# Kernel tuning notes

Hardware: AMD Instinct MI355X
Metric: run time of the kernel (lower is better)

The kernel has to match this reference:

```python
import jax, jax.numpy as jnp
import numpy as np

B, N, C, H, D = 1, 256, 128, 4, 32  # batch, n_res, c_z, heads, head_dim
LN_EPS = 1e-5


def setup_inputs() -> dict:
    key = jax.random.key(0)
    ks = jax.random.split(key, 10)
    s = 0.02
    return {
        "act": jax.random.normal(ks[0], (B, N, N, C), dtype=jnp.float32),
        "mask": jnp.ones((B, N, N), dtype=jnp.float32),
        "ln_g": jnp.ones((C,), dtype=jnp.float32),
        "ln_b": jnp.zeros((C,), dtype=jnp.float32),
        "w2d": jax.random.normal(ks[1], (C, H), dtype=jnp.float32) * s,
        "wq": jax.random.normal(ks[2], (C, H, D), dtype=jnp.float32) * s,
        "wk": jax.random.normal(ks[3], (C, H, D), dtype=jnp.float32) * s,
        "wv": jax.random.normal(ks[4], (C, H, D), dtype=jnp.float32) * s,
        "wg": jax.random.normal(ks[5], (C, H, D), dtype=jnp.float32) * s,
        "bg": jnp.ones((H, D), dtype=jnp.float32),
        "wo": jax.random.normal(ks[6], (H, D, C), dtype=jnp.float32) * s,
        "bo": jnp.zeros((C,), dtype=jnp.float32),
    }


def reference(act, mask, ln_g, ln_b, w2d, wq, wk, wv, wg, bg, wo, bo):
    # LayerNorm over channel dim
    mu = jnp.mean(act, axis=-1, keepdims=True)
    var = jnp.mean(jnp.square(act - mu), axis=-1, keepdims=True)
    x = (act - mu) * jax.lax.rsqrt(var + LN_EPS) * ln_g + ln_b  # [B,N,N,C]

    # mask bias: [B, I, 1, 1, K]
    mask_bias = (1e9 * (mask - 1.0))[:, :, None, None, :]
    # nonbatched pair bias: [B, 1, H, Q, K]
    nb_bias = jnp.einsum('bqkc,ch->bhqk', x, w2d)[:, None]

    scale = 1.0 / jnp.sqrt(jnp.asarray(D, dtype=x.dtype))
    q = jnp.einsum('bijc,chd->bijhd', x, wq) * scale  # [B,I,Q,H,D]
    k = jnp.einsum('bijc,chd->bijhd', x, wk)
    v = jnp.einsum('bijc,chd->bijhd', x, wv)

    logits = jnp.einsum('biqhd,bikhd->bihqk', q, k) + mask_bias + nb_bias
    a = jax.nn.softmax(logits, axis=-1)  # [B,I,H,Q,K]
    o = jnp.einsum('bihqk,bikhd->biqhd', a, v)  # [B,I,Q,H,D]

    g = jax.nn.sigmoid(jnp.einsum('bijc,chd->bijhd', x, wg) + bg)
    o = o * g
    out = jnp.einsum('biqhd,hdc->biqc', o, wo) + bo  # [B,N,N,C]
    return out
```

## Files before the change

kernel.cpp:

```cpp
#include <hip/hip_runtime.h>

#define QK_SCALE 0.17677669529663689f

typedef float f4 __attribute__((ext_vector_type(4)));
typedef short bf16x8 __attribute__((ext_vector_type(8)));
typedef float f32x4 __attribute__((ext_vector_type(4)));
typedef unsigned short us4 __attribute__((ext_vector_type(4)));
typedef unsigned int u32x2 __attribute__((ext_vector_type(2)));
typedef unsigned int u32x4 __attribute__((ext_vector_type(4)));

__device__ __forceinline__ unsigned short f2bf(float x){
  unsigned int u = __float_as_uint(x);
  u += 0x7fffu + ((u >> 16) & 1u);
  return (unsigned short)(u >> 16);
}
__device__ __forceinline__ float bf2f(unsigned short h){
  return __uint_as_float(((unsigned int)h) << 16);
}
__device__ __forceinline__ unsigned int cvtpk(float lo, float hi){
  unsigned int r;
  asm volatile("v_cvt_pk_bf16_f32 %0, %1, %2" : "=v"(r) : "v"(lo), "v"(hi));
  return r;
}
__device__ __forceinline__ f32x4 mfma16(bf16x8 a, bf16x8 b, f32x4 c){
  return __builtin_amdgcn_mfma_f32_16x16x32_bf16(a, b, c, 0, 0, 0);
}
__device__ __forceinline__ void gload_lds16(const void* g, void* s){
  __builtin_amdgcn_global_load_lds(
      (const __attribute__((address_space(1))) unsigned int*)g,
      (__attribute__((address_space(3))) unsigned int*)s, 16, 0, 0);
}

__global__ __launch_bounds__(256)
void k_prep(const float* __restrict__ wq, const float* __restrict__ wk,
            const float* __restrict__ wv, const float* __restrict__ wg,
            const float* __restrict__ wo, unsigned short* __restrict__ pk)
{
  const int m = blockIdx.x;
  const float* W = (m==0)? wq : (m==1)? wk : (m==2)? wv : (m==3)? wg : wo;
  const float scale = (m==0)? QK_SCALE : 1.0f;
  unsigned short* dst = pk + (long)m * 32768;
  for (int ent = threadIdx.x; ent < 2048; ent += 256){
    const int l = ent & 63, ktn = ent >> 6;
    const int kt = ktn & 3, nt = ktn >> 2;
    unsigned short* ph = dst + ((nt*4 + kt)*2 + 0)*512 + l*8;
    unsigned short* pl = dst + ((nt*4 + kt)*2 + 1)*512 + l*8;
    #pragma unroll
    for (int e = 0; e < 8; ++e){
      const int row = kt*32 + (l>>4)*8 + e;
      const int col = nt*16 + (l&15);
      float v = W[row*128 + col] * scale;
      unsigned short hh = f2bf(v);
      ph[e] = hh;
      pl[e] = f2bf(v - bf2f(hh));
    }
  }
}

__global__ __launch_bounds__(512, 4)
void k_proj(const float* __restrict__ act, const float* __restrict__ ln_g,
            const float* __restrict__ ln_b, const float* __restrict__ w2d,
            const unsigned short* __restrict__ pk, const float* __restrict__ bg,
            unsigned short* __restrict__ qf, unsigned short* __restrict__ kf,
            unsigned short* __restrict__ vt, unsigned short* __restrict__ gg,
            unsigned short* __restrict__ b2dh)
{
  __shared__ unsigned short afr[8*4*2*512];
  __shared__ unsigned short sc[4*640];
  const int t = threadIdx.x, w = t>>6, l = t&63, g16 = l>>4, c = l&15;
  const long p0 = (long)blockIdx.x * 128;
  const int bi = (int)(p0 >> 8);
  const int qb0 = (int)(p0 & 255);
  const int row = w*16 + c;

  {
    const float* ap = act + (p0 + row)*128;
    f4 xv[4][2];
    #pragma unroll
    for (int kt = 0; kt < 4; ++kt){
      xv[kt][0] = *(const f4*)(ap + kt*32 + g16*8);
      xv[kt][1] = *(const f4*)(ap + kt*32 + g16*8 + 4);
    }
    float s = 0.f, s2 = 0.f;
    #pragma unroll
    for (int kt = 0; kt < 4; ++kt)
      #pragma unroll
      for (int u = 0; u < 2; ++u)
        #pragma unroll
        for (int e = 0; e < 4; ++e){
          float x = xv[kt][u][e]; s += x; s2 += x*x;
        }
    s += __shfl_xor(s,16); s2 += __shfl_xor(s2,16);
    s += __shfl_xor(s,32); s2 += __shfl_xor(s2,32);
    const float mu = s*(1.f/128.f);
    const float iv = rsqrtf(fmaxf(s2*(1.f/128.f)-mu*mu,0.f)+1e-5f);

    float pb0=0.f, pb1=0.f, pb2=0.f, pb3=0.f;
    #pragma unroll
    for (int kt = 0; kt < 4; ++kt){
      bf16x8 hv, lv;
      #pragma unroll
      for (int u = 0; u < 2; ++u){
        const int cb = kt*32 + g16*8 + u*4;
        f4 lg = *(const f4*)(ln_g + cb);
        f4 lb = *(const f4*)(ln_b + cb);
        #pragma unroll
        for (int e0 = 0; e0 < 4; ++e0){
          float vv = (xv[kt][u][e0]-mu)*iv*lg[e0] + lb[e0];
          f4 wp = *(const f4*)(w2d + (cb+e0)*4);
          pb0 += vv*wp[0]; pb1 += vv*wp[1]; pb2 += vv*wp[2]; pb3 += vv*wp[3];
          unsigned short hh = f2bf(vv);
          hv[u*4+e0] = (short)hh;
          lv[u*4+e0] = (short)f2bf(vv - bf2f(hh));
        }
      }
      *(bf16x8*)&afr[((w*4+kt)*2+0)*512 + l*8] = hv;
      *(bf16x8*)&afr[((w*4+kt)*2+1)*512 + l*8] = lv;
    }
    pb0 += __shfl_xor(pb0,16); pb1 += __shfl_xor(pb1,16);
    pb2 += __shfl_xor(pb2,16); pb3 += __shfl_xor(pb3,16);
    pb0 += __shfl_xor(pb0,32); pb1 += __shfl_xor(pb1,32);
    pb2 += __shfl_xor(pb2,32); pb3 += __shfl_xor(pb3,32);
    const float pbsel = (g16==0)? pb0 : (g16==1)? pb1 : (g16==2)? pb2 : pb3;
    b2dh[g16*65536 + (int)p0 + row] = f2bf(pbsel);
  }
  __syncthreads();

  #pragma unroll
  for (int pass = 0; pass < 2; ++pass){
    bf16x8 bh0[4], bl0[4], bh1[4], bl1[4];
    { const int ntg = w*4 + pass*2;
      #pragma unroll
      for (int kt = 0; kt < 4; ++kt){
        bh0[kt] = *(const bf16x8*)(pk + ((ntg*4+kt)*2+0)*512 + l*8);
        bl0[kt] = *(const bf16x8*)(pk + ((ntg*4+kt)*2+1)*512 + l*8);
        bh1[kt] = *(const bf16x8*)(pk + (((ntg+1)*4+kt)*2+0)*512 + l*8);
        bl1[kt] = *(const bf16x8*)(pk + (((ntg+1)*4+kt)*2+1)*512 + l*8);
      } }
    for (int rt = 0; rt < 8; ++rt){
      bf16x8 ah[4], al[4];
      #pragma unroll
      for (int kt = 0; kt < 4; ++kt){
        ah[kt] = *(const bf16x8*)&afr[((rt*4+kt)*2+0)*512 + l*8];
        al[kt] = *(const bf16x8*)&afr[((rt*4+kt)*2+1)*512 + l*8];
      }
      f32x4 a0 = {0.f,0.f,0.f,0.f}, a1 = {0.f,0.f,0.f,0.f};
      #pragma unroll
      for (int kt = 0; kt < 4; ++kt){
        a0 = mfma16(ah[kt], bh0[kt], a0);
        a1 = mfma16(ah[kt], bh1[kt], a1);
        a0 = mfma16(ah[kt], bl0[kt], a0);
        a1 = mfma16(ah[kt], bl1[kt], a1);
        a0 = mfma16(al[kt], bh0[kt], a0);
        a1 = mfma16(al[kt], bh1[kt], a1);
      }
      if (w < 4){
        unsigned short* scw = sc + w*640;
        #pragma unroll
        for (int j = 0; j < 4; ++j){
          scw[(g16*4+j)*40 + c]      = f2bf(a0[j]);
          scw[(g16*4+j)*40 + 16 + c] = f2bf(a1[j]);
        }
        asm volatile("" ::: "memory");
        bf16x8 fr = *(const bf16x8*)&scw[c*40 + g16*8];
        const int head = (w&1)*2 + pass;
        unsigned short* dst = (w < 2) ? qf : kf;
        *(bf16x8*)&dst[(((long)bi*4+head)*16 + (qb0>>4) + rt)*512 + l*8] = fr;
        asm volatile("" ::: "memory");
      } else if (w < 6){
        const int ntv0 = (w-4)*4 + pass*2;
        const int kv = qb0 + rt*16 + g16*4;
        #pragma unroll
        for (int np = 0; np < 2; ++np){
          const int colg = (ntv0+np)*16 + c;
          const int head = colg >> 5, d = colg & 31;
          f32x4 aa = np ? a1 : a0;
          us4 v4;
          #pragma unroll
          for (int j = 0; j < 4; ++j) v4[j] = f2bf(aa[j]);
          const int vb = (d*512 + kv*2) ^ ((d&7)<<4);
          *(us4*)((char*)vt + ((long)bi*4+head)*16384 + vb) = v4;
        }
      } else {
        const int colb = (w-6)*64 + pass*32;
        const int row0 = (int)p0 + rt*16 + g16*4;
        const float bg0 = bg[colb + c];
        const float bg1 = bg[colb + 16 + c];
        #pragma unroll
        for (int j = 0; j < 4; ++j){
          float g0 = 1.f/(1.f + __expf(-(a0[j] + bg0)));
          float g1 = 1.f/(1.f + __expf(-(a1[j] + bg1)));
          gg[(row0+j)*128 + colb + c]      = f2bf(g0);
          gg[(row0+j)*128 + colb + 16 + c] = f2bf(g1);
        }
      }
    }
  }
}

__global__ __launch_bounds__(512, 4)
void k_attn(const unsigned short* __restrict__ qf, const unsigned short* __restrict__ kfg,
            const unsigned short* __restrict__ vt, const unsigned short* __restrict__ gg,
            const unsigned short* __restrict__ b2dh, const float* __restrict__ mask,
            unsigned short* __restrict__ obf)
{
  __shared__ unsigned short k_s[16*512];
  __shared__ unsigned short v_s[8192];
  __shared__ float mb_s[256];
  const int t = threadIdx.x, w = t>>6, l = t&63, g16 = l>>4, c = l&15;
  const int bi = blockIdx.x >> 2, h = blockIdx.x & 3;
  const int base = (bi*4+h)*8192;

  if (t < 256) mb_s[t] = 1e9f * (mask[bi*256 + t] - 1.0f);
  const bf16x8 qfr0 = *(const bf16x8*)(qf + base + (w*2+0)*512 + l*8);
  const bf16x8 qfr1 = *(const bf16x8*)(qf + base + (w*2+1)*512 + l*8);
  gload_lds16(kfg + base + (w*2+0)*512 + l*8, k_s + (w*2+0)*512);
  gload_lds16(kfg + base + (w*2+1)*512 + l*8, k_s + (w*2+1)*512);
  gload_lds16(vt  + base + (w*2+0)*512 + l*8, v_s + (w*2+0)*512);
  gload_lds16(vt  + base + (w*2+1)*512 + l*8, v_s + (w*2+1)*512);
  asm volatile("s_waitcnt vmcnt(2) lgkmcnt(0)" ::: "memory");
  __builtin_amdgcn_s_barrier();

  const int swz = (c&7)<<4;
  const int a0 = (((l & 16) << 1) | c) << 2;
  const int a1 = a0 + 64;
  const bool hi = (l >= 32);

  #pragma unroll
  for (int im = 0; im < 2; ++im){
    const int q0 = w*32 + im*16;
    const bf16x8 qfr = im ? qfr1 : qfr0;
    const unsigned short* bq = b2dh + h*65536 + (q0 + c)*256 + g16*4;
    f32x4 sa[16];
    __builtin_amdgcn_s_setprio(1);
    #pragma unroll
    for (int nt = 0; nt < 16; ++nt){
      const us4 bh4 = *(const us4*)(bq + nt*16);
      const f4 mv = *(const f4*)&mb_s[nt*16 + g16*4];
      f32x4 ci;
      ci[0] = mv[0] + bf2f(bh4[0]);
      ci[1] = mv[1] + bf2f(bh4[1]);
      ci[2] = mv[2] + bf2f(bh4[2]);
      ci[3] = mv[3] + bf2f(bh4[3]);
      sa[nt] = mfma16(*(const bf16x8*)(k_s + nt*512 + l*8), qfr, ci);
    }
    __builtin_amdgcn_s_setprio(0);
    f32x4 sv = {0.f,0.f,0.f,0.f};
    #pragma unroll
    for (int nt = 0; nt < 16; ++nt){
      #pragma unroll
      for (int j = 0; j < 4; ++j){
        float e = exp2f(sa[nt][j] * 1.44269504f);
        sa[nt][j] = e;
        sv[j] += e;
      }
    }
    float sum = (sv[0]+sv[1]) + (sv[2]+sv[3]);
    sum += __shfl_xor(sum, 16);
    sum += __shfl_xor(sum, 32);
    const float inv = 1.f / sum;
    if (im == 0){
      asm volatile("s_waitcnt vmcnt(0)" ::: "memory");
      __builtin_amdgcn_s_barrier();
    }
    f32x4 oa0 = {0.f,0.f,0.f,0.f}, oa1 = {0.f,0.f,0.f,0.f};
    #pragma unroll
    for (int kt = 0; kt < 8; ++kt){
      const unsigned X0 = cvtpk(sa[2*kt][0],   sa[2*kt][1]);
      const unsigned X1 = cvtpk(sa[2*kt][2],   sa[2*kt][3]);
      const unsigned Y0 = cvtpk(sa[2*kt+1][0], sa[2*kt+1][1]);
      const unsigned Y1 = cvtpk(sa[2*kt+1][2], sa[2*kt+1][3]);
      const int pX0 = __builtin_amdgcn_ds_bpermute(a0, (int)X0);
      const int pY0 = __builtin_amdgcn_ds_bpermute(a0, (int)Y0);
      const int pX1 = __builtin_amdgcn_ds_bpermute(a0, (int)X1);
      const int pY1 = __builtin_amdgcn_ds_bpermute(a0, (int)Y1);
      const int pX2 = __builtin_amdgcn_ds_bpermute(a1, (int)X0);
      const int pY2 = __builtin_amdgcn_ds_bpermute(a1, (int)Y0);
      const int pX3 = __builtin_amdgcn_ds_bpermute(a1, (int)X1);
      const int pY3 = __builtin_amdgcn_ds_bpermute(a1, (int)Y1);
      u32x4 pu;
      pu[0] = (unsigned)(hi ? pY0 : pX0);
      pu[1] = (unsigned)(hi ? pY1 : pX1);
      pu[2] = (unsigned)(hi ? pY2 : pX2);
      pu[3] = (unsigned)(hi ? pY3 : pX3);
      const bf16x8 pf = __builtin_bit_cast(bf16x8, pu);
      const int vb0 = ((c*512      + kt*64 + g16*16) ^ swz);
      const int vb1 = (((16+c)*512 + kt*64 + g16*16) ^ swz);
      oa0 = mfma16(*(const bf16x8*)((const char*)v_s + vb0), pf, oa0);
      oa1 = mfma16(*(const bf16x8*)((const char*)v_s + vb1), pf, oa1);
    }
    const int row = bi*256 + q0 + c;
    us4 gv0 = *(const us4*)&gg[row*128 + h*32 + g16*4];
    us4 gv1 = *(const us4*)&gg[row*128 + h*32 + 16 + g16*4];
    u32x2 o0, o1;
    o0[0] = cvtpk(oa0[0]*inv*bf2f(gv0[0]), oa0[1]*inv*bf2f(gv0[1]));
    o0[1] = cvtpk(oa0[2]*inv*bf2f(gv0[2]), oa0[3]*inv*bf2f(gv0[3]));
    o1[0] = cvtpk(oa1[0]*inv*bf2f(gv1[0]), oa1[1]*inv*bf2f(gv1[1]));
    o1[1] = cvtpk(oa1[2]*inv*bf2f(gv1[2]), oa1[3]*inv*bf2f(gv1[3]));
    *(u32x2*)&obf[row*128 + h*32 + g16*4]      = o0;
    *(u32x2*)&obf[row*128 + h*32 + 16 + g16*4] = o1;
  }
}

__global__ __launch_bounds__(512, 4)
void k_out(const unsigned short* __restrict__ obf, const unsigned short* __restrict__ pko,
           const float* __restrict__ bo, float* __restrict__ out)
{
  __shared__ unsigned short afr[32*512];
  const int t = threadIdx.x, w = t>>6, l = t&63, g16 = l>>4, c = l&15;
  const long p0 = (long)blockIdx.x * 128;

  #pragma unroll
  for (int u = 0; u < 4; ++u){
    const int pr = w*4 + u;
    const int rt = pr >> 2, kt = pr & 3;
    gload_lds16(obf + (p0 + rt*16 + c)*128 + kt*32 + g16*8, afr + pr*512);
  }
  asm volatile("s_waitcnt vmcnt(0)" ::: "memory");
  __syncthreads();

  bf16x8 bh[4], bl[4];
  #pragma unroll
  for (int kt = 0; kt < 4; ++kt){
    bh[kt] = *(const bf16x8*)(pko + ((w*4+kt)*2+0)*512 + l*8);
    bl[kt] = *(const bf16x8*)(pko + ((w*4+kt)*2+1)*512 + l*8);
  }
  const float bov = bo[w*16 + c];
  for (int rt = 0; rt < 8; ++rt){
    f32x4 a0 = {bov, bov, bov, bov};
    #pragma unroll
    for (int kt = 0; kt < 4; ++kt){
      bf16x8 af = *(const bf16x8*)&afr[(rt*4+kt)*512 + l*8];
      a0 = mfma16(af, bh[kt], a0);
      a0 = mfma16(af, bl[kt], a0);
    }
    const int row0 = (int)p0 + rt*16 + g16*4;
    #pragma unroll
    for (int j = 0; j < 4; ++j)
      out[(row0+j)*128 + w*16 + c] = a0[j];
  }
}

extern "C" void kernel_launch(void* const* d_in, const int* in_sizes, int n_in,
                              void* d_out, int out_size, void* d_ws, size_t ws_size,
                              hipStream_t stream) {
  const float* act  = (const float*)d_in[0];
  const float* mask = (const float*)d_in[1];
  const float* ln_g = (const float*)d_in[2];
  const float* ln_b = (const float*)d_in[3];
  const float* w2d  = (const float*)d_in[4];
  const float* wq   = (const float*)d_in[5];
  const float* wk   = (const float*)d_in[6];
  const float* wv   = (const float*)d_in[7];
  const float* wg   = (const float*)d_in[8];
  const float* bg   = (const float*)d_in[9];
  const float* wo   = (const float*)d_in[10];
  const float* bo   = (const float*)d_in[11];
  float* out = (float*)d_out;

  char* ws = (char*)d_ws;
  unsigned short* qf   = (unsigned short*)(ws);
  unsigned short* kfb  = (unsigned short*)(ws + 16777216L);
  unsigned short* vt   = (unsigned short*)(ws + 33554432L);
  unsigned short* gg   = (unsigned short*)(ws + 50331648L);
  unsigned short* obf  = (unsigned short*)(ws + 67108864L);
  unsigned short* b2dh = (unsigned short*)(ws + 83886080L);
  unsigned short* pk   = (unsigned short*)(ws + 84934656L);

  k_prep<<<5, 256, 0, stream>>>(wq, wk, wv, wg, wo, pk);
  k_proj<<<512, 512, 0, stream>>>(act, ln_g, ln_b, w2d, pk, bg,
                                  qf, kfb, vt, gg, b2dh);
  k_attn<<<1024, 512, 0, stream>>>(qf, kfb, vt, gg, b2dh, mask, obf);
  k_out<<<512, 512, 0, stream>>>(obf, pk + 4*32768, bo, out);
}
```

Measured before the change: 111.5 us.

## Hold K and V fragments in registers instead of LDS in attention kernel

The attention kernel stops staging K, V and the mask bias in shared memory. Each wave now loads all 16 K fragments and 16 V fragments directly from global memory into registers and reads the mask per use. The block shrinks to 256 threads, with each wave handling four 16-query tiles instead of two. This removes LDS traffic and the block barriers, but each wave loads the full K/V redundantly from global/L2, register pressure rises sharply, and the launch bound drops occupancy to 2.

```diff
diff --git a/kernel.cpp b/kernel.cpp
--- a/kernel.cpp
+++ b/kernel.cpp
@@ -198,51 +198,52 @@
   }
 }
 
-__global__ __launch_bounds__(512, 4)
+__global__ __launch_bounds__(256, 2)
 void k_attn(const unsigned short* __restrict__ qf, const unsigned short* __restrict__ kfg,
             const unsigned short* __restrict__ vt, const unsigned short* __restrict__ gg,
             const unsigned short* __restrict__ b2dh, const float* __restrict__ mask,
             unsigned short* __restrict__ obf)
 {
-  __shared__ unsigned short k_s[16*512];
-  __shared__ unsigned short v_s[8192];
-  __shared__ float mb_s[256];
   const int t = threadIdx.x, w = t>>6, l = t&63, g16 = l>>4, c = l&15;
   const int bi = blockIdx.x >> 2, h = blockIdx.x & 3;
   const int base = (bi*4+h)*8192;
-
-  if (t < 256) mb_s[t] = 1e9f * (mask[bi*256 + t] - 1.0f);
-  const bf16x8 qfr0 = *(const bf16x8*)(qf + base + (w*2+0)*512 + l*8);
-  const bf16x8 qfr1 = *(const bf16x8*)(qf + base + (w*2+1)*512 + l*8);
-  gload_lds16(kfg + base + (w*2+0)*512 + l*8, k_s + (w*2+0)*512);
-  gload_lds16(kfg + base + (w*2+1)*512 + l*8, k_s + (w*2+1)*512);
-  gload_lds16(vt  + base + (w*2+0)*512 + l*8, v_s + (w*2+0)*512);
-  gload_lds16(vt  + base + (w*2+1)*512 + l*8, v_s + (w*2+1)*512);
-  asm volatile("s_waitcnt vmcnt(2) lgkmcnt(0)" ::: "memory");
-  __builtin_amdgcn_s_barrier();
-
   const int swz = (c&7)<<4;
+
+  bf16x8 kfr[16];
+  #pragma unroll
+  for (int nt = 0; nt < 16; ++nt)
+    kfr[nt] = *(const bf16x8*)(kfg + base + nt*512 + l*8);
+  bf16x8 vfr0[8], vfr1[8];
+  #pragma unroll
+  for (int kt = 0; kt < 8; ++kt){
+    const int vb0 = ((c*512      + kt*64 + g16*16) ^ swz);
+    const int vb1 = (((16+c)*512 + kt*64 + g16*16) ^ swz);
+    vfr0[kt] = *(const bf16x8*)((const char*)(vt + base) + vb0);
+    vfr1[kt] = *(const bf16x8*)((const char*)(vt + base) + vb1);
+  }
+  const float* mrow = mask + bi*256;
+
   const int a0 = (((l & 16) << 1) | c) << 2;
   const int a1 = a0 + 64;
   const bool hi = (l >= 32);
 
   #pragma unroll
-  for (int im = 0; im < 2; ++im){
-    const int q0 = w*32 + im*16;
-    const bf16x8 qfr = im ? qfr1 : qfr0;
+  for (int im = 0; im < 4; ++im){
+    const int q0 = w*64 + im*16;
+    const bf16x8 qfr = *(const bf16x8*)(qf + base + (q0>>4)*512 + l*8);
     const unsigned short* bq = b2dh + h*65536 + (q0 + c)*256 + g16*4;
     f32x4 sa[16];
     __builtin_amdgcn_s_setprio(1);
     #pragma unroll
     for (int nt = 0; nt < 16; ++nt){
       const us4 bh4 = *(const us4*)(bq + nt*16);
-      const f4 mv = *(const f4*)&mb_s[nt*16 + g16*4];
+      const f4 mv = *(const f4*)(mrow + nt*16 + g16*4);
       f32x4 ci;
-      ci[0] = mv[0] + bf2f(bh4[0]);
-      ci[1] = mv[1] + bf2f(bh4[1]);
-      ci[2] = mv[2] + bf2f(bh4[2]);
-      ci[3] = mv[3] + bf2f(bh4[3]);
-      sa[nt] = mfma16(*(const bf16x8*)(k_s + nt*512 + l*8), qfr, ci);
+      ci[0] = 1e9f*(mv[0]-1.f) + bf2f(bh4[0]);
+      ci[1] = 1e9f*(mv[1]-1.f) + bf2f(bh4[1]);
+      ci[2] = 1e9f*(mv[2]-1.f) + bf2f(bh4[2]);
+      ci[3] = 1e9f*(mv[3]-1.f) + bf2f(bh4[3]);
+      sa[nt] = mfma16(kfr[nt], qfr, ci);
     }
     __builtin_amdgcn_s_setprio(0);
     f32x4 sv = {0.f,0.f,0.f,0.f};
@@ -259,10 +260,6 @@
     sum += __shfl_xor(sum, 16);
     sum += __shfl_xor(sum, 32);
     const float inv = 1.f / sum;
-    if (im == 0){
-      asm volatile("s_waitcnt vmcnt(0)" ::: "memory");
-      __builtin_amdgcn_s_barrier();
-    }
     f32x4 oa0 = {0.f,0.f,0.f,0.f}, oa1 = {0.f,0.f,0.f,0.f};
     #pragma unroll
     for (int kt = 0; kt < 8; ++kt){
@@ -284,10 +281,8 @@
       pu[2] = (unsigned)(hi ? pY2 : pX2);
       pu[3] = (unsigned)(hi ? pY3 : pX3);
       const bf16x8 pf = __builtin_bit_cast(bf16x8, pu);
-      const int vb0 = ((c*512      + kt*64 + g16*16) ^ swz);
-      const int vb1 = (((16+c)*512 + kt*64 + g16*16) ^ swz);
-      oa0 = mfma16(*(const bf16x8*)((const char*)v_s + vb0), pf, oa0);
-      oa1 = mfma16(*(const bf16x8*)((const char*)v_s + vb1), pf, oa1);
+      oa0 = mfma16(vfr0[kt], pf, oa0);
+      oa1 = mfma16(vfr1[kt], pf, oa1);
     }
     const int row = bi*256 + q0 + c;
     us4 gv0 = *(const us4*)&gg[row*128 + h*32 + g16*4];
@@ -370,6 +365,6 @@
   k_prep<<<5, 256, 0, stream>>>(wq, wk, wv, wg, wo, pk);
   k_proj<<<512, 512, 0, stream>>>(act, ln_g, ln_b, w2d, pk, bg,
                                   qf, kfb, vt, gg, b2dh);
-  k_attn<<<1024, 512, 0, stream>>>(qf, kfb, vt, gg, b2dh, mask, obf);
+  k_attn<<<1024, 256, 0, stream>>>(qf, kfb, vt, gg, b2dh, mask, obf);
   k_out<<<512, 512, 0, stream>>>(obf, pk + 4*32768, bo, out);
 }
```

Result: slower. 134.3 us (+20.5%).
